# Kernel optimization log

Measured on AMD Instinct MI355X. Metric: run time of the kernel, lower is better.

Reference implementation:

```python
import jax, jax.numpy as jnp
import numpy as np

POOL_H, POOL_W = 7, 7
NUM_LEVELS = 4


def _crop_and_resize(image, boxes, box_indices, pool_h, pool_w):
    """Faithful tf.image.crop_and_resize (bilinear, extrapolation_value=0).

    image: [B, H, W, C]; boxes: [M, 4] (y1,x1,y2,x2) normalized; box_indices: [M] int32.
    Returns [M, pool_h, pool_w, C].
    """
    H, W = image.shape[1], image.shape[2]
    dt = image.dtype
    y1, x1, y2, x2 = boxes[:, 0], boxes[:, 1], boxes[:, 2], boxes[:, 3]
    gi = jnp.arange(pool_h, dtype=dt)
    gj = jnp.arange(pool_w, dtype=dt)
    # sample coordinates in source-image pixel space: [M, ph] / [M, pw]
    in_y = y1[:, None] * (H - 1) + gi[None, :] * ((y2 - y1) * (H - 1) / (pool_h - 1))[:, None]
    in_x = x1[:, None] * (W - 1) + gj[None, :] * ((x2 - x1) * (W - 1) / (pool_w - 1))[:, None]
    valid_y = (in_y >= 0) & (in_y <= H - 1)
    valid_x = (in_x >= 0) & (in_x <= W - 1)
    fy = jnp.floor(in_y)
    fx = jnp.floor(in_x)
    ty = jnp.clip(fy, 0, H - 1).astype(jnp.int32)
    by = jnp.minimum(ty + 1, H - 1)
    lx = jnp.clip(fx, 0, W - 1).astype(jnp.int32)
    rx = jnp.minimum(lx + 1, W - 1)
    wy = (in_y - fy)[:, :, None, None]   # [M, ph, 1, 1]
    wx = (in_x - fx)[:, None, :, None]   # [M, 1, pw, 1]
    bi = box_indices[:, None, None]
    tl = image[bi, ty[:, :, None], lx[:, None, :]]  # [M, ph, pw, C]
    tr = image[bi, ty[:, :, None], rx[:, None, :]]
    bl = image[bi, by[:, :, None], lx[:, None, :]]
    br = image[bi, by[:, :, None], rx[:, None, :]]
    top = tl + (tr - tl) * wx
    bot = bl + (br - bl) * wx
    out = top + (bot - top) * wy
    mask = (valid_y[:, :, None] & valid_x[:, None, :])[..., None]
    return jnp.where(mask, out, jnp.zeros((), dt))


def setup_inputs() -> dict:
    key = jax.random.key(0)
    ks = jax.random.split(key, 8)
    B, N, C = 2, 1000, 256
    sizes = [256, 128, 64, 32]
    yx1 = jax.random.uniform(ks[0], (B, N, 2), dtype=jnp.float32) * 0.8
    hw = jax.random.uniform(ks[1], (B, N, 2), dtype=jnp.float32) * 0.2 + 0.02
    boxes = jnp.concatenate([yx1, jnp.clip(yx1 + hw, 0.0, 1.0)], axis=-1)  # (y1,x1,y2,x2)
    fms = [jax.random.normal(ks[2 + l], (B, s, s, C), dtype=jnp.float32) for l, s in enumerate(sizes)]
    box_fpn_level = jax.random.randint(ks[6], (B, N), 1, NUM_LEVELS + 1, dtype=jnp.int32)
    return {"boxes": boxes, "fm0": fms[0], "fm1": fms[1], "fm2": fms[2], "fm3": fms[3],
            "box_fpn_level": box_fpn_level}


def reference(boxes, fm0, fm1, fm2, fm3, box_fpn_level):
    feature_maps = [fm0, fm1, fm2, fm3]
    B, N = boxes.shape[0], boxes.shape[1]
    C = fm0.shape[-1]
    flat_boxes = boxes.reshape(B * N, 4)
    flat_level = box_fpn_level.reshape(B * N)
    batch_idx = (jnp.arange(B * N, dtype=jnp.int32) // N).astype(jnp.int32)
    pooled = jnp.zeros((B * N, POOL_H, POOL_W, C), dtype=fm0.dtype)
    for l, fm in enumerate(feature_maps):
        p = _crop_and_resize(fm, flat_boxes, batch_idx, POOL_H, POOL_W)
        sel = (flat_level == l + 1)[:, None, None, None]
        pooled = jnp.where(sel, p, pooled)
    pooled = pooled.reshape(B, N, POOL_H, POOL_W, C)
    # TF concatenates per-level crops then dynamic_partitions by batch: within
    # each batch, boxes end up grouped by FPN level (stable within a level).
    order = jnp.argsort(box_fpn_level, axis=1, stable=True)  # [B, N]
    out = jnp.take_along_axis(pooled, order[:, :, None, None, None], axis=1)
    return out  # [B, MAX_OUTPUT_SIZE(=N), ph, pw, C]
```

## Files before the change

### kernel.cpp

```cpp
#include <hip/hip_runtime.h>

#define POOL 7
#define PP   (POOL * POOL)

__global__ void compute_order_kernel(const int* __restrict__ levels,
                                     int* __restrict__ dst, int N) {
    __shared__ int lvl[1024];
    const int b = blockIdx.x;
    const int n = threadIdx.x;
    const int* L = levels + (size_t)b * N;
    if (n < N) lvl[n] = L[n];
    __syncthreads();
    if (n < N) {
        const int my = lvl[n];
        int pos = 0;
        for (int m = 0; m < N; ++m) {
            const int lm = lvl[m];
            pos += (int)((lm < my) | ((lm == my) & (m < n)));
        }
        dst[(size_t)b * N + n] = pos;
    }
}

__global__ __launch_bounds__(256) void roi_align_kernel(
    const float* __restrict__ boxes,
    const float* __restrict__ fm0, const float* __restrict__ fm1,
    const float* __restrict__ fm2, const float* __restrict__ fm3,
    const int* __restrict__ levels, const int* __restrict__ dst,
    float* __restrict__ out, int N, int C) {

    const int box_flat = blockIdx.x;
    const int wave = threadIdx.x >> 6;
    const int lane = threadIdx.x & 63;
    const int b = box_flat / N;

    const int lv = levels[box_flat] - 1;
    const float* fm; int S;
    if      (lv == 0) { fm = fm0; S = 256; }
    else if (lv == 1) { fm = fm1; S = 128; }
    else if (lv == 2) { fm = fm2; S = 64;  }
    else              { fm = fm3; S = 32;  }

    const double y1 = (double)boxes[(size_t)box_flat * 4 + 0];
    const double x1 = (double)boxes[(size_t)box_flat * 4 + 1];
    const double y2 = (double)boxes[(size_t)box_flat * 4 + 2];
    const double x2 = (double)boxes[(size_t)box_flat * 4 + 3];

    const double Hm1 = (double)(S - 1);
    const double sy = (y2 - y1) * Hm1 / (double)(POOL - 1);
    const double sx = (x2 - x1) * Hm1 / (double)(POOL - 1);
    const double oy = y1 * Hm1;
    const double ox = x1 * Hm1;

    const int pos = dst[box_flat];
    const float* fmb  = fm  + (size_t)b * S * S * C;
    float*       outb = out + ((size_t)b * N + pos) * PP * C;

    for (int pq = wave; pq < PP; pq += 4) {
        const int gi = pq / POOL;
        const int gj = pq - gi * POOL;

        const double in_y = oy + (double)gi * sy;
        const double in_x = ox + (double)gj * sx;
        const bool valid = (in_y >= 0.0) && (in_y <= Hm1) &&
                           (in_x >= 0.0) && (in_x <= Hm1);

        const double fy = floor(in_y);
        const double fx = floor(in_x);
        const float wy = (float)(in_y - fy);
        const float wx = (float)(in_x - fx);

        const int ty = (int)fmin(fmax(fy, 0.0), Hm1);
        const int by = min(ty + 1, S - 1);
        const int lx = (int)fmin(fmax(fx, 0.0), Hm1);
        const int rx = min(lx + 1, S - 1);

        const float* rowT = fmb + (size_t)ty * S * C;
        const float* rowB = fmb + (size_t)by * S * C;
        float* op = outb + (size_t)pq * C;

        for (int c = lane * 4; c < C; c += 256) {
            const float4 tl = *(const float4*)(rowT + (size_t)lx * C + c);
            const float4 tr = *(const float4*)(rowT + (size_t)rx * C + c);
            const float4 bl = *(const float4*)(rowB + (size_t)lx * C + c);
            const float4 br = *(const float4*)(rowB + (size_t)rx * C + c);

            float4 o;
            {
                float top = tl.x + (tr.x - tl.x) * wx;
                float bot = bl.x + (br.x - bl.x) * wx;
                o.x = top + (bot - top) * wy;
                top = tl.y + (tr.y - tl.y) * wx;
                bot = bl.y + (br.y - bl.y) * wx;
                o.y = top + (bot - top) * wy;
                top = tl.z + (tr.z - tl.z) * wx;
                bot = bl.z + (br.z - bl.z) * wx;
                o.z = top + (bot - top) * wy;
                top = tl.w + (tr.w - tl.w) * wx;
                bot = bl.w + (br.w - bl.w) * wx;
                o.w = top + (bot - top) * wy;
            }
            if (!valid) { o.x = 0.0f; o.y = 0.0f; o.z = 0.0f; o.w = 0.0f; }
            *(float4*)(op + c) = o;
        }
    }
}

extern "C" void kernel_launch(void* const* d_in, const int* in_sizes, int n_in,
                              void* d_out, int out_size, void* d_ws, size_t ws_size,
                              hipStream_t stream) {
    const float* boxes  = (const float*)d_in[0];
    const float* fm0    = (const float*)d_in[1];
    const float* fm1    = (const float*)d_in[2];
    const float* fm2    = (const float*)d_in[3];
    const float* fm3    = (const float*)d_in[4];
    const int*   levels = (const int*)d_in[5];
    float* out = (float*)d_out;

    const int BN = in_sizes[5];
    const int C  = out_size / (BN * PP);
    const int B  = in_sizes[1] / (256 * 256 * C);
    const int N  = BN / B;

    int* dst = (int*)d_ws;

    compute_order_kernel<<<B, 1024, 0, stream>>>(levels, dst, N);
    roi_align_kernel<<<BN, 256, 0, stream>>>(boxes, fm0, fm1, fm2, fm3,
                                             levels, dst, out, N, C);
}
```

Before: 300.0 us.

## Split ROI work by output row across grid, unroll columns with single-wave blocks

Each block was one 256-thread box walking all 49 bins. Now it is a single 64-lane wave handling one output row of one box, with the grid extended to BN x 7 and the seven columns unrolled. Row coordinates and row pointers are computed once per block, and invalid bins skip their loads. The intent is more blocks, more independent loads in flight per wave, and less repeated index math. The costs are seven times more tiny blocks and an assumption that C equals 256, since the channel loop was removed.

Measured after the change: 298.9 us. Within noise of the previous version (-0.4%).

```diff
diff --git a/kernel.cpp b/kernel.cpp
--- a/kernel.cpp
+++ b/kernel.cpp
@@ -22,7 +22,7 @@
     }
 }
 
-__global__ __launch_bounds__(256) void roi_align_kernel(
+__global__ __launch_bounds__(64) void roi_align_kernel(
     const float* __restrict__ boxes,
     const float* __restrict__ fm0, const float* __restrict__ fm1,
     const float* __restrict__ fm2, const float* __restrict__ fm3,
@@ -30,8 +30,8 @@
     float* __restrict__ out, int N, int C) {
 
     const int box_flat = blockIdx.x;
-    const int wave = threadIdx.x >> 6;
-    const int lane = threadIdx.x & 63;
+    const int gi   = blockIdx.y;
+    const int lane = threadIdx.x;
     const int b = box_flat / N;
 
     const int lv = levels[box_flat] - 1;
@@ -49,60 +49,58 @@
     const double Hm1 = (double)(S - 1);
     const double sy = (y2 - y1) * Hm1 / (double)(POOL - 1);
     const double sx = (x2 - x1) * Hm1 / (double)(POOL - 1);
-    const double oy = y1 * Hm1;
-    const double ox = x1 * Hm1;
+
+    const double in_y = y1 * Hm1 + (double)gi * sy;
+    const bool vy = (in_y >= 0.0) && (in_y <= Hm1);
+    const double fy = floor(in_y);
+    const float  wy = (float)(in_y - fy);
+    const int ty = (int)fmin(fmax(fy, 0.0), Hm1);
+    const int by = min(ty + 1, S - 1);
+
+    const float* fmb  = fm + (size_t)b * S * S * C;
+    const float* rowT = fmb + (size_t)ty * S * C;
+    const float* rowB = fmb + (size_t)by * S * C;
 
     const int pos = dst[box_flat];
-    const float* fmb  = fm  + (size_t)b * S * S * C;
-    float*       outb = out + ((size_t)b * N + pos) * PP * C;
+    float* orow = out + (((size_t)b * N + pos) * PP + (size_t)gi * POOL) * C
+                      + lane * 4;
 
-    for (int pq = wave; pq < PP; pq += 4) {
-        const int gi = pq / POOL;
-        const int gj = pq - gi * POOL;
+    const double ox = x1 * Hm1;
+    const int c = lane * 4;
 
-        const double in_y = oy + (double)gi * sy;
+#pragma unroll
+    for (int gj = 0; gj < POOL; ++gj) {
         const double in_x = ox + (double)gj * sx;
-        const bool valid = (in_y >= 0.0) && (in_y <= Hm1) &&
-                           (in_x >= 0.0) && (in_x <= Hm1);
+        const bool valid = vy && (in_x >= 0.0) && (in_x <= Hm1);
 
-        const double fy = floor(in_y);
-        const double fx = floor(in_x);
-        const float wy = (float)(in_y - fy);
-        const float wx = (float)(in_x - fx);
+        float4 o;
+        if (valid) {
+            const double fx = floor(in_x);
+            const float  wx = (float)(in_x - fx);
+            const int lx = (int)fmin(fmax(fx, 0.0), Hm1);
+            const int rx = min(lx + 1, S - 1);
 
-        const int ty = (int)fmin(fmax(fy, 0.0), Hm1);
-        const int by = min(ty + 1, S - 1);
-        const int lx = (int)fmin(fmax(fx, 0.0), Hm1);
-        const int rx = min(lx + 1, S - 1);
-
-        const float* rowT = fmb + (size_t)ty * S * C;
-        const float* rowB = fmb + (size_t)by * S * C;
-        float* op = outb + (size_t)pq * C;
-
-        for (int c = lane * 4; c < C; c += 256) {
             const float4 tl = *(const float4*)(rowT + (size_t)lx * C + c);
             const float4 tr = *(const float4*)(rowT + (size_t)rx * C + c);
             const float4 bl = *(const float4*)(rowB + (size_t)lx * C + c);
             const float4 br = *(const float4*)(rowB + (size_t)rx * C + c);
 
-            float4 o;
-            {
-                float top = tl.x + (tr.x - tl.x) * wx;
-                float bot = bl.x + (br.x - bl.x) * wx;
-                o.x = top + (bot - top) * wy;
-                top = tl.y + (tr.y - tl.y) * wx;
-                bot = bl.y + (br.y - bl.y) * wx;
-                o.y = top + (bot - top) * wy;
-                top = tl.z + (tr.z - tl.z) * wx;
-                bot = bl.z + (br.z - bl.z) * wx;
-                o.z = top + (bot - top) * wy;
-                top = tl.w + (tr.w - tl.w) * wx;
-                bot = bl.w + (br.w - bl.w) * wx;
-                o.w = top + (bot - top) * wy;
-            }
-            if (!valid) { o.x = 0.0f; o.y = 0.0f; o.z = 0.0f; o.w = 0.0f; }
-            *(float4*)(op + c) = o;
+            float top = tl.x + (tr.x - tl.x) * wx;
+            float bot = bl.x + (br.x - bl.x) * wx;
+            o.x = top + (bot - top) * wy;
+            top = tl.y + (tr.y - tl.y) * wx;
+            bot = bl.y + (br.y - bl.y) * wx;
+            o.y = top + (bot - top) * wy;
+            top = tl.z + (tr.z - tl.z) * wx;
+            bot = bl.z + (br.z - bl.z) * wx;
+            o.z = top + (bot - top) * wy;
+            top = tl.w + (tr.w - tl.w) * wx;
+            bot = bl.w + (br.w - bl.w) * wx;
+            o.w = top + (bot - top) * wy;
+        } else {
+            o.x = 0.0f; o.y = 0.0f; o.z = 0.0f; o.w = 0.0f;
         }
+        *(float4*)(orow + (size_t)gj * C) = o;
     }
 }
 
@@ -125,6 +123,6 @@
     int* dst = (int*)d_ws;
 
     compute_order_kernel<<<B, 1024, 0, stream>>>(levels, dst, N);
-    roi_align_kernel<<<BN, 256, 0, stream>>>(boxes, fm0, fm1, fm2, fm3,
-                                             levels, dst, out, N, C);
+    roi_align_kernel<<<dim3(BN, POOL), 64, 0, stream>>>(
+        boxes, fm0, fm1, fm2, fm3, levels, dst, out, N, C);
 }
```
